# Kernel tuning notes

Measured on AMD Instinct MI355X. Metric: run time of the kernel, lower is better.

Reference implementation:

```python
import jax, jax.numpy as jnp
import numpy as np


def _lap_mul(A, x):
    # L @ x with L = D^{-1/2} A D^{-1/2}, D = diag(rowsum(A))
    d = 1.0 / jnp.sqrt(jnp.sum(A, axis=-1))  # [N]
    return d[:, None] * (A @ (d[:, None] * x))


def setup_inputs() -> dict:
    key = jax.random.key(0)
    k1, k2, k3, k4, k5, k6 = jax.random.split(key, 6)
    N, D_IN, D_OUT = 4096, 128, 128
    x = jax.random.normal(k1, (N, D_IN), dtype=jnp.float32)
    A = jax.random.uniform(k2, (N, N), dtype=jnp.float32)
    # linear params stored as [in, out] (apply via x @ W + b)
    s1 = 1.0 / np.sqrt(D_IN)
    W1 = jax.random.uniform(k3, (D_IN, D_OUT), minval=-s1, maxval=s1, dtype=jnp.float32)
    b1 = jax.random.uniform(k4, (D_OUT,), minval=-s1, maxval=s1, dtype=jnp.float32)
    W2 = jax.random.uniform(k5, (D_IN, D_OUT), minval=-s1, maxval=s1, dtype=jnp.float32)
    b2 = jax.random.uniform(k6, (D_OUT,), minval=-s1, maxval=s1, dtype=jnp.float32)
    return {"x": x, "A": A, "W1": W1, "b1": b1, "W2": W2, "b2": b2, "sigma": 1, "k": 4}


def reference(x, A, W1, b1, W2, b2, sigma, k):
    # first graph conv + linear1 + leaky relu
    z = _lap_mul(A, x) @ W1 + b1            # [N, d_out]
    z = jax.nn.leaky_relu(z, negative_slope=0.1)

    # pairwise Euclidean distance (efficient cdist form, same math as the
    # original broadcasted (z_i - z_j)**2 sum, without the d x N x N blowup)
    sq = jnp.sum(z * z, axis=-1)            # [N]
    d2 = sq[:, None] + sq[None, :] - 2.0 * (z @ z.T)
    d2 = jnp.maximum(d2, 0.0)
    S = jnp.sqrt(d2 + 1e-10)                # [N, N]
    S = jnp.exp(-S / (2.0 * sigma))

    # double-argsort rank -> keep top-k per row (emulates original masking)
    order = jnp.argsort(-S, axis=-1)
    ranks = jnp.argsort(order, axis=-1)
    S = jnp.where(ranks < k, S, 0.0)

    A2 = S + A
    out = _lap_mul(A2, x) @ W2 + b2         # [N, d_out]
    return out
```

## Files before the change

kernel.cpp:

```cpp
#include <hip/hip_runtime.h>
#include <cstdint>
#include <cstddef>

#define NN 4096
#define DD 128

using short8 = __attribute__((ext_vector_type(8))) short;
using f32x4  = __attribute__((ext_vector_type(4))) float;
typedef unsigned long long u64;

typedef __attribute__((address_space(1))) void gvoid;
typedef __attribute__((address_space(3))) void lvoid;

__device__ __forceinline__ void async16(const void* g, void* l) {
  __builtin_amdgcn_global_load_lds((gvoid*)g, (lvoid*)l, 16, 0, 0);
}

__device__ __forceinline__ float dec_f(const void* p) {
  if (!p) return 1.0f;
  int b = *(const int*)p;
  return (b >= 0 && b < 1000000) ? (float)b : __int_as_float(b);
}
__device__ __forceinline__ int dec_i(const void* p) {
  if (!p) return 4;
  int b = *(const int*)p;
  return (b >= 0 && b < 1000000) ? b : (int)__int_as_float(b);
}

__device__ __forceinline__ unsigned short f2bf(float f) {
  union { float f; unsigned int u; } v; v.f = f;
  unsigned int u = v.u;
  unsigned int r = (u + 0x7fffu + ((u >> 16) & 1u)) >> 16;
  return (unsigned short)r;
}

__device__ __forceinline__ void ins4(u64 (&l)[4], u64 k) {
#pragma unroll
  for (int t = 0; t < 4; ++t) {
    u64 old = l[t];
    bool bt = k < old;
    l[t] = bt ? k : old;
    k = bt ? old : k;
  }
}

template <int ROWS, int KC, int NTHR>
__device__ __forceinline__ void stage2(const unsigned short* src, int row0, int kb,
                                       unsigned short* dst, int tid, int stride) {
  const int CPR = KC / 8;
  const int ITER = (ROWS * CPR) / NTHR;
#pragma unroll
  for (int t = 0; t < ITER; ++t) {
    int id = tid + t * NTHR;
    int r = id / CPR;
    int p = id % CPR;
    int lc = p ^ (r & 7);
    const void* g = src + (size_t)(row0 + r) * stride + kb + lc * 8;
    async16(g, dst + (size_t)(id & ~63) * 8);
  }
}

template <int CPR>
__device__ __forceinline__ short8 fragN(const unsigned short* t, int row, int ch) {
  return *(const short8*)(t + (size_t)(row * CPR + (ch ^ (row & 7))) * 8);
}

__global__ __launch_bounds__(256) void k_rowsum_scale(
    const float* __restrict__ A, float* __restrict__ rowsumA,
    float* __restrict__ dvec, unsigned short* __restrict__ Ah) {
  int row = blockIdx.x;
  int tid = threadIdx.x;
  const float4* Arow = (const float4*)(A + (size_t)row * NN);
  float s = 0.f;
#pragma unroll
  for (int l = 0; l < 4; ++l) {
    int idx = tid + l * 256;
    float4 v = Arow[idx];
    s += (v.x + v.y) + (v.z + v.w);
    ushort4 h = {f2bf(v.x), f2bf(v.y), f2bf(v.z), f2bf(v.w)};
    *(ushort4*)(Ah + (size_t)row * NN + idx * 4) = h;
  }
  __shared__ float red[256];
  red[tid] = s;
  __syncthreads();
  if (tid < 64) {
    s = red[tid] + red[tid + 64] + red[tid + 128] + red[tid + 192];
#pragma unroll
    for (int off = 32; off > 0; off >>= 1) s += __shfl_down(s, off, 64);
    if (tid == 0) { rowsumA[row] = s; dvec[row] = rsqrtf(s); }
  }
}

__global__ __launch_bounds__(256) void k_xwt(
    const float* __restrict__ x, const float* __restrict__ scale,
    const float* __restrict__ W, float* __restrict__ U,
    unsigned short* __restrict__ UTh) {
  int r0 = blockIdx.x * 16, tid = threadIdx.x;
  int tr = tid >> 4, tc = tid & 15;
  __shared__ float Xs[16 * 132];
  __shared__ float Ws[32 * 128];
  __shared__ unsigned short Ts[128 * 16];
  __shared__ float ssc[16];
  if (tid < 16) ssc[tid] = scale[r0 + tid];
  __syncthreads();
#pragma unroll
  for (int l = 0; l < 2; ++l) {
    int idx = tid + l * 256;
    int r = idx >> 5, c4 = (idx & 31) << 2;
    float4 xv = *(const float4*)(x + (size_t)(r0 + r) * DD + c4);
    float sc = ssc[r];
    float4 o = {sc * xv.x, sc * xv.y, sc * xv.z, sc * xv.w};
    *(float4*)(Xs + r * 132 + c4) = o;
  }
  float acc[8];
#pragma unroll
  for (int u = 0; u < 8; ++u) acc[u] = 0.f;
  for (int t0 = 0; t0 < 128; t0 += 32) {
    __syncthreads();
#pragma unroll
    for (int l = 0; l < 4; ++l) {
      int idx = tid + l * 256;
      int tt = idx >> 5, c4 = (idx & 31) << 2;
      *(float4*)(Ws + tt * 128 + c4) = *(const float4*)(W + (size_t)(t0 + tt) * DD + c4);
    }
    __syncthreads();
#pragma unroll 8
    for (int tt = 0; tt < 32; ++tt) {
      float g = Xs[tr * 132 + t0 + tt];
      float4 w0 = *(const float4*)(Ws + tt * 128 + tc * 8);
      float4 w1 = *(const float4*)(Ws + tt * 128 + tc * 8 + 4);
      acc[0] = fmaf(g, w0.x, acc[0]); acc[1] = fmaf(g, w0.y, acc[1]);
      acc[2] = fmaf(g, w0.z, acc[2]); acc[3] = fmaf(g, w0.w, acc[3]);
      acc[4] = fmaf(g, w1.x, acc[4]); acc[5] = fmaf(g, w1.y, acc[5]);
      acc[6] = fmaf(g, w1.z, acc[6]); acc[7] = fmaf(g, w1.w, acc[7]);
    }
  }
  if (U) {
    size_t off = (size_t)(r0 + tr) * DD + tc * 8;
    float4 o0 = {acc[0], acc[1], acc[2], acc[3]};
    float4 o1 = {acc[4], acc[5], acc[6], acc[7]};
    *(float4*)(U + off) = o0;
    *(float4*)(U + off + 4) = o1;
  }
#pragma unroll
  for (int j = 0; j < 8; ++j) Ts[(tc * 8 + j) * 16 + tr] = f2bf(acc[j]);
  __syncthreads();
  {
    int row = tid >> 1, h = tid & 1;
    *(short8*)(UTh + (size_t)row * NN + r0 + h * 8) = *(const short8*)(Ts + row * 16 + h * 8);
  }
}

__global__ __launch_bounds__(256) void k_mxwt(
    const u64* __restrict__ pkey, const float* __restrict__ rowsumA,
    const float* __restrict__ x, const float* __restrict__ W,
    float* __restrict__ sval, int* __restrict__ sidx, float* __restrict__ d2vec,
    float* __restrict__ U, unsigned short* __restrict__ UTh,
    const void* kptr, const void* sigptr) {
  int r0 = blockIdx.x * 16, tid = threadIdx.x;
  int tr = tid >> 4, tc = tid & 15;
  __shared__ float Xs[16 * 132];
  __shared__ float Ws[32 * 128];
  __shared__ unsigned short Ts[128 * 16];
  __shared__ u64 mk[256][4];
  __shared__ float ds[16];

  {
    int r = tid >> 4, p = tid & 15;
    const u64* src = pkey + ((size_t)(r0 + r) * 16 + p) * 4;
    ulonglong2 k0 = *(const ulonglong2*)src;
    ulonglong2 k1 = *(const ulonglong2*)(src + 2);
    mk[tid][0] = k0.x; mk[tid][1] = k0.y; mk[tid][2] = k1.x; mk[tid][3] = k1.y;
  }
  __syncthreads();
#pragma unroll
  for (int s = 8; s > 0; s >>= 1) {
    int p = tid & 15;
    if (p < s) {
      u64 b[4] = {mk[tid][0], mk[tid][1], mk[tid][2], mk[tid][3]};
#pragma unroll
      for (int q = 0; q < 4; ++q) ins4(b, mk[tid + s][q]);
      mk[tid][0] = b[0]; mk[tid][1] = b[1]; mk[tid][2] = b[2]; mk[tid][3] = b[3];
    }
    __syncthreads();
  }
  if ((tid & 15) == 0) {
    int rl = tid >> 4;
    int r = r0 + rl;
    int kk = dec_i(kptr); kk = kk < 1 ? 1 : (kk > 4 ? 4 : kk);
    float inv2s = 0.5f / dec_f(sigptr);
    float srw = 0.f;
#pragma unroll
    for (int s = 0; s < 4; ++s) {
      if (s < kk) {
        u64 key = mk[tid][s];
        float d2 = __uint_as_float((unsigned)(key >> 32));
        float S = __expf(-sqrtf(d2 + 1e-10f) * inv2s);
        sval[r * 8 + s] = S;
        sidx[r * 8 + s] = (int)(key & 0xffffffffu);
        srw += S;
      }
    }
    float dd = rsqrtf(rowsumA[r] + srw);
    d2vec[r] = dd;
    ds[rl] = dd;
  }
  __syncthreads();

#pragma unroll
  for (int l = 0; l < 2; ++l) {
    int idx = tid + l * 256;
    int r = idx >> 5, c4 = (idx & 31) << 2;
    float4 xv = *(const float4*)(x + (size_t)(r0 + r) * DD + c4);
    float sc = ds[r];
    float4 o = {sc * xv.x, sc * xv.y, sc * xv.z, sc * xv.w};
    *(float4*)(Xs + r * 132 + c4) = o;
  }
  float acc[8];
#pragma unroll
  for (int u = 0; u < 8; ++u) acc[u] = 0.f;
  for (int t0 = 0; t0 < 128; t0 += 32) {
    __syncthreads();
#pragma unroll
    for (int l = 0; l < 4; ++l) {
      int idx = tid + l * 256;
      int tt = idx >> 5, c4 = (idx & 31) << 2;
      *(float4*)(Ws + tt * 128 + c4) = *(const float4*)(W + (size_t)(t0 + tt) * DD + c4);
    }
    __syncthreads();
#pragma unroll 8
    for (int tt = 0; tt < 32; ++tt) {
      float g = Xs[tr * 132 + t0 + tt];
      float4 w0 = *(const float4*)(Ws + tt * 128 + tc * 8);
      float4 w1 = *(const float4*)(Ws + tt * 128 + tc * 8 + 4);
      acc[0] = fmaf(g, w0.x, acc[0]); acc[1] = fmaf(g, w0.y, acc[1]);
      acc[2] = fmaf(g, w0.z, acc[2]); acc[3] = fmaf(g, w0.w, acc[3]);
      acc[4] = fmaf(g, w1.x, acc[4]); acc[5] = fmaf(g, w1.y, acc[5]);
      acc[6] = fmaf(g, w1.z, acc[6]); acc[7] = fmaf(g, w1.w, acc[7]);
    }
  }
  {
    size_t off = (size_t)(r0 + tr) * DD + tc * 8;
    float4 o0 = {acc[0], acc[1], acc[2], acc[3]};
    float4 o1 = {acc[4], acc[5], acc[6], acc[7]};
    *(float4*)(U + off) = o0;
    *(float4*)(U + off + 4) = o1;
  }
#pragma unroll
  for (int j = 0; j < 8; ++j) Ts[(tc * 8 + j) * 16 + tr] = f2bf(acc[j]);
  __syncthreads();
  {
    int row = tid >> 1, h = tid & 1;
    *(short8*)(UTh + (size_t)row * NN + r0 + h * 8) = *(const short8*)(Ts + row * 16 + h * 8);
  }
}

template <int SPLIT>
__global__ __launch_bounds__(256) void k_gemm_bf16(
    const unsigned short* __restrict__ Ah, const unsigned short* __restrict__ Bh,
    float* __restrict__ G) {
  __shared__ __align__(16) unsigned short As_h[128 * 64];
  __shared__ __align__(16) unsigned short Bs_h[128 * 64];

  int bx = blockIdx.x;
  int mt = bx / SPLIT, sp = bx % SPLIT;
  int m0 = mt * 128;
  const int KLEN = NN / SPLIT;
  int ks = sp * KLEN;
  int tid = threadIdx.x, lane = tid & 63, w = tid >> 6;
  int wm = w >> 1, wn = w & 1;
  int l15 = lane & 15, quad = lane >> 4;

  f32x4 acc[4][4];
#pragma unroll
  for (int a = 0; a < 4; ++a)
#pragma unroll
    for (int b = 0; b < 4; ++b) acc[a][b] = (f32x4){0.f, 0.f, 0.f, 0.f};

  for (int kt = 0; kt < KLEN; kt += 64) {
    int kb = ks + kt;
    __syncthreads();
    stage2<128, 64, 256>(Ah, m0, kb, As_h, tid, NN);
    stage2<128, 64, 256>(Bh, 0, kb, Bs_h, tid, NN);
    __syncthreads();
#pragma unroll
    for (int k0 = 0; k0 < 64; k0 += 32) {
      int ch = (k0 >> 3) + quad;
      short8 a_h[4], b_h[4];
#pragma unroll
      for (int f = 0; f < 4; ++f) {
        a_h[f] = fragN<8>(As_h, wm * 64 + f * 16 + l15, ch);
        b_h[f] = fragN<8>(Bs_h, wn * 64 + f * 16 + l15, ch);
      }
#pragma unroll
      for (int fm = 0; fm < 4; ++fm)
#pragma unroll
        for (int fn = 0; fn < 4; ++fn)
          acc[fm][fn] = __builtin_amdgcn_mfma_f32_16x16x32_bf16(a_h[fm], b_h[fn], acc[fm][fn], 0, 0, 0);
    }
  }
  float* Gp = G + (size_t)sp * NN * DD;
#pragma unroll
  for (int fm = 0; fm < 4; ++fm) {
    int rb = m0 + wm * 64 + fm * 16 + quad * 4;
#pragma unroll
    for (int fn = 0; fn < 4; ++fn) {
      int c = wn * 64 + fn * 16 + l15;
#pragma unroll
      for (int i = 0; i < 4; ++i)
        Gp[(size_t)(rb + i) * DD + c] = acc[fm][fn][i];
    }
  }
}

template <int NP>
__global__ __launch_bounds__(256) void k_red(
    const float* __restrict__ G, const float* __restrict__ dvec,
    const float* __restrict__ bvec, int leaky,
    float* __restrict__ Out, unsigned short* __restrict__ zh,
    float* __restrict__ sqout,
    const float* __restrict__ Usp, const float* __restrict__ sval,
    const int* __restrict__ sidx, const void* kptr) {
  int r0 = blockIdx.x * 16;
  int tid = threadIdx.x;
  int tr = tid >> 4, tc = tid & 15;
  int r = r0 + tr;
  size_t off = (size_t)r * DD + tc * 8;
  __shared__ float red[256];

  float acc[8];
#pragma unroll
  for (int u = 0; u < 8; ++u) acc[u] = 0.f;
#pragma unroll
  for (int p = 0; p < NP; ++p) {
    const float* gp = G + (size_t)p * NN * DD + off;
    float4 g0 = *(const float4*)gp;
    float4 g1 = *(const float4*)(gp + 4);
    acc[0] += g0.x; acc[1] += g0.y; acc[2] += g0.z; acc[3] += g0.w;
    acc[4] += g1.x; acc[5] += g1.y; acc[6] += g1.z; acc[7] += g1.w;
  }
  if (sidx != nullptr) {
    int kk = dec_i(kptr); kk = kk < 1 ? 1 : (kk > 4 ? 4 : kk);
    for (int t = 0; t < kk; ++t) {
      float sv = sval[r * 8 + t];
      int id = sidx[r * 8 + t];
      const float* vr = Usp + (size_t)id * DD + tc * 8;
      float4 w0 = *(const float4*)vr;
      float4 w1 = *(const float4*)(vr + 4);
      acc[0] = fmaf(sv, w0.x, acc[0]); acc[1] = fmaf(sv, w0.y, acc[1]);
      acc[2] = fmaf(sv, w0.z, acc[2]); acc[3] = fmaf(sv, w0.w, acc[3]);
      acc[4] = fmaf(sv, w1.x, acc[4]); acc[5] = fmaf(sv, w1.y, acc[5]);
      acc[6] = fmaf(sv, w1.z, acc[6]); acc[7] = fmaf(sv, w1.w, acc[7]);
    }
  }
  float d = dvec[r];
  float4 b0 = *(const float4*)(bvec + tc * 8);
  float4 b1 = *(const float4*)(bvec + tc * 8 + 4);
  float bb[8] = {b0.x, b0.y, b0.z, b0.w, b1.x, b1.y, b1.z, b1.w};
  float o[8];
#pragma unroll
  for (int u = 0; u < 8; ++u) {
    float v = fmaf(d, acc[u], bb[u]);
    if (leaky) v = v > 0.f ? v : 0.1f * v;
    o[u] = v;
  }
  if (Out) {
    float4 o0 = {o[0], o[1], o[2], o[3]};
    float4 o1 = {o[4], o[5], o[6], o[7]};
    *(float4*)(Out + off) = o0;
    *(float4*)(Out + off + 4) = o1;
  }
  if (zh) {
    ushort4 h0 = {f2bf(o[0]), f2bf(o[1]), f2bf(o[2]), f2bf(o[3])};
    ushort4 h1 = {f2bf(o[4]), f2bf(o[5]), f2bf(o[6]), f2bf(o[7])};
    *(ushort4*)(zh + off) = h0;
    *(ushort4*)(zh + off + 4) = h1;
  }
  if (sqout != nullptr) {
    float p = 0.f;
#pragma unroll
    for (int u = 0; u < 8; ++u) p = fmaf(o[u], o[u], p);
    red[tid] = p;
    __syncthreads();
    if (tc == 0) {
      float s = 0.f;
#pragma unroll
      for (int i = 0; i < 16; ++i) s += red[tr * 16 + i];
      sqout[r] = s;
    }
  }
}

__global__ __launch_bounds__(512, 8) void k_scores(
    const unsigned short* __restrict__ Zh,
    const float* __restrict__ sq, u64* __restrict__ pkey) {
  __shared__ __align__(16) unsigned short Am[64 * 128];
  __shared__ __align__(16) unsigned short Bj[64 * 128];
  float* Stile = (float*)&Bj[0];
  u64* mv = (u64*)&Am[0];

  int bx = blockIdx.x;
  int mt = bx >> 4, jp = bx & 15;
  int m0 = mt * 64, j0 = jp * 256;
  int tid = threadIdx.x, lane = tid & 63, w = tid >> 6;
  int wm = w >> 2, wn = w & 3;
  int l15 = lane & 15, quad = lane >> 4;

  stage2<64, 128, 512>(Zh, m0, 0, Am, tid, DD);

  int srow = tid >> 3;
  int sc = tid & 7;
  float sqi_r = sq[m0 + srow];

  u64 lst[4];
#pragma unroll
  for (int s = 0; s < 4; ++s) lst[s] = ~0ull;

  for (int jt = 0; jt < 4; ++jt) {
    int jrow0 = j0 + jt * 64;
    __syncthreads();
    stage2<64, 128, 512>(Zh, jrow0, 0, Bj, tid, DD);
    __syncthreads();

    f32x4 acc[2];
    acc[0] = (f32x4){0.f, 0.f, 0.f, 0.f};
    acc[1] = (f32x4){0.f, 0.f, 0.f, 0.f};
#pragma unroll
    for (int kc = 0; kc < 4; ++kc) {
      int ch = kc * 4 + quad;
      short8 ah0 = fragN<16>(Am, wm * 32 + l15, ch);
      short8 ah1 = fragN<16>(Am, wm * 32 + 16 + l15, ch);
      short8 bh  = fragN<16>(Bj, wn * 16 + l15, ch);
      acc[0] = __builtin_amdgcn_mfma_f32_16x16x32_bf16(ah0, bh, acc[0], 0, 0, 0);
      acc[1] = __builtin_amdgcn_mfma_f32_16x16x32_bf16(ah1, bh, acc[1], 0, 0, 0);
    }
    __syncthreads();

    {
      int c = wn * 16 + l15;
      float sqjv = sq[jrow0 + c];
      int cslot = c >> 2, cw = c & 3;
#pragma unroll
      for (int fm = 0; fm < 2; ++fm) {
        int rb = wm * 32 + fm * 16 + quad * 4;
#pragma unroll
        for (int i = 0; i < 4; ++i) {
          int r = rb + i;
          Stile[r * 64 + ((cslot ^ (r & 7)) << 2) + cw] = fmaf(-2.f, acc[fm][i], sqjv);
        }
      }
    }
    __syncthreads();

#pragma unroll
    for (int q = 0; q < 2; ++q) {
      int slot = sc * 2 + q;
      float4 kv = *(const float4*)(Stile + srow * 64 + ((slot ^ (srow & 7)) << 2));
      int jb = jrow0 + sc * 8 + q * 4;
      float ke[4] = {kv.x, kv.y, kv.z, kv.w};
#pragma unroll
      for (int e = 0; e < 4; ++e) {
        float v = fmaxf(sqi_r + ke[e], 0.f);
        ins4(lst, ((u64)__float_as_uint(v) << 32) | (unsigned)(jb + e));
      }
    }
  }

  __syncthreads();
#pragma unroll
  for (int s = 0; s < 4; ++s) mv[tid * 4 + s] = lst[s];
  __syncthreads();
  if (tid < 64) {
    u64 best[4] = {~0ull, ~0ull, ~0ull, ~0ull};
    for (int g = 0; g < 8; ++g) {
      int src = tid * 8 + g;
#pragma unroll
      for (int s = 0; s < 4; ++s) ins4(best, mv[src * 4 + s]);
    }
#pragma unroll
    for (int s = 0; s < 4; ++s)
      pkey[((size_t)(m0 + tid) * 16 + jp) * 4 + s] = best[s];
  }
}

extern "C" void kernel_launch(void* const* d_in, const int* in_sizes, int n_in,
                              void* d_out, int out_size, void* d_ws, size_t ws_size,
                              hipStream_t stream) {
  const float* x  = (const float*)d_in[0];
  const float* A  = (const float*)d_in[1];
  const float* W1 = (const float*)d_in[2];
  const float* b1 = (const float*)d_in[3];
  const float* W2 = (const float*)d_in[4];
  const float* b2 = (const float*)d_in[5];
  const void* sig = (n_in > 6) ? d_in[6] : nullptr;
  const void* kp  = (n_in > 7) ? d_in[7] : nullptr;

  float* ws = (float*)d_ws;
  float* rowsumA = ws;
  float* dvec    = ws + 4096;
  float* d2vec   = ws + 8192;
  float* sqv     = ws + 12288;
  float* sval    = ws + 16384;
  int*   sidx    = (int*)(ws + 49152);
  u64*   pkey    = (u64*)(ws + 81920);
  unsigned short* Zh  = (unsigned short*)(ws + 606208);
  float* U       = ws + 868352;
  unsigned short* UTh = (unsigned short*)(ws + 1392640);
  unsigned short* Ah  = (unsigned short*)(ws + 1654784);
  float* G       = ws + 10043392;

  const size_t F16 = 10043392 + 16 * 524288;
  int split16 = (ws_size >= F16 * 4);

  k_rowsum_scale<<<4096, 256, 0, stream>>>(A, rowsumA, dvec, Ah);
  k_xwt<<<256, 256, 0, stream>>>(x, dvec, W1, nullptr, UTh);
  if (split16) {
    k_gemm_bf16<16><<<512, 256, 0, stream>>>(Ah, UTh, G);
    k_red<16><<<256, 256, 0, stream>>>(G, dvec, b1, 1, nullptr, Zh, sqv,
                                       nullptr, nullptr, nullptr, nullptr);
  } else {
    k_gemm_bf16<4><<<128, 256, 0, stream>>>(Ah, UTh, G);
    k_red<4><<<256, 256, 0, stream>>>(G, dvec, b1, 1, nullptr, Zh, sqv,
                                      nullptr, nullptr, nullptr, nullptr);
  }
  k_scores<<<1024, 512, 0, stream>>>(Zh, sqv, pkey);
  k_mxwt<<<256, 256, 0, stream>>>(pkey, rowsumA, x, W2, sval, sidx, d2vec,
                                  U, UTh, kp, sig);
  if (split16) {
    k_gemm_bf16<16><<<512, 256, 0, stream>>>(Ah, UTh, G);
    k_red<16><<<256, 256, 0, stream>>>(G, d2vec, b2, 0, (float*)d_out, nullptr, nullptr,
                                       U, sval, sidx, kp);
  } else {
    k_gemm_bf16<4><<<128, 256, 0, stream>>>(Ah, UTh, G);
    k_red<4><<<256, 256, 0, stream>>>(G, d2vec, b2, 0, (float*)d_out, nullptr, nullptr,
                                      U, sval, sidx, kp);
  }
}
```

Measured before the change: 199.0 us.

## Fuse split-K reduction into GEMM via last-block counter and prune top-k inserts

Merges the split-K partial-sum reduction and epilogue (scaling, bias, leaky relu, bf16 output, squared norms, sparse top-k contribution) into the GEMM kernel. The last block per row tile, detected with an atomic counter, does the reduction, which removes two kernel launches and their gaps. Counters are zeroed inside the row-sum kernel. The scores kernel also skips top-4 insertion when a candidate exceeds the current fourth-best key. The tradeoff is that the reduction now runs on only 32 blocks, serialised behind the tail of the GEMM.

```diff
diff --git a/kernel.cpp b/kernel.cpp
--- a/kernel.cpp
+++ b/kernel.cpp
@@ -67,9 +67,11 @@
 
 __global__ __launch_bounds__(256) void k_rowsum_scale(
     const float* __restrict__ A, float* __restrict__ rowsumA,
-    float* __restrict__ dvec, unsigned short* __restrict__ Ah) {
+    float* __restrict__ dvec, unsigned short* __restrict__ Ah,
+    int* __restrict__ cnt) {
   int row = blockIdx.x;
   int tid = threadIdx.x;
+  if (row == 0 && tid < 128) cnt[tid] = 0;
   const float4* Arow = (const float4*)(A + (size_t)row * NN);
   float s = 0.f;
 #pragma unroll
@@ -256,11 +258,18 @@
 }
 
 template <int SPLIT>
-__global__ __launch_bounds__(256) void k_gemm_bf16(
+__global__ __launch_bounds__(256) void k_gemm_fused(
     const unsigned short* __restrict__ Ah, const unsigned short* __restrict__ Bh,
-    float* __restrict__ G) {
+    float* __restrict__ G, int* __restrict__ cnt,
+    const float* __restrict__ dvec, const float* __restrict__ bvec, int leaky,
+    float* __restrict__ Out, unsigned short* __restrict__ zh,
+    float* __restrict__ sqout,
+    const float* __restrict__ Usp, const float* __restrict__ sval,
+    const int* __restrict__ sidx, const void* kptr) {
   __shared__ __align__(16) unsigned short As_h[128 * 64];
   __shared__ __align__(16) unsigned short Bs_h[128 * 64];
+  __shared__ float redsh[256];
+  __shared__ int islast;
 
   int bx = blockIdx.x;
   int mt = bx / SPLIT, sp = bx % SPLIT;
@@ -299,94 +308,95 @@
           acc[fm][fn] = __builtin_amdgcn_mfma_f32_16x16x32_bf16(a_h[fm], b_h[fn], acc[fm][fn], 0, 0, 0);
     }
   }
-  float* Gp = G + (size_t)sp * NN * DD;
-#pragma unroll
-  for (int fm = 0; fm < 4; ++fm) {
-    int rb = m0 + wm * 64 + fm * 16 + quad * 4;
-#pragma unroll
-    for (int fn = 0; fn < 4; ++fn) {
-      int c = wn * 64 + fn * 16 + l15;
-#pragma unroll
-      for (int i = 0; i < 4; ++i)
-        Gp[(size_t)(rb + i) * DD + c] = acc[fm][fn][i];
-    }
-  }
-}
-
-template <int NP>
-__global__ __launch_bounds__(256) void k_red(
-    const float* __restrict__ G, const float* __restrict__ dvec,
-    const float* __restrict__ bvec, int leaky,
-    float* __restrict__ Out, unsigned short* __restrict__ zh,
-    float* __restrict__ sqout,
-    const float* __restrict__ Usp, const float* __restrict__ sval,
-    const int* __restrict__ sidx, const void* kptr) {
-  int r0 = blockIdx.x * 16;
-  int tid = threadIdx.x;
+  {
+    float* Gp = G + (size_t)sp * NN * DD;
+#pragma unroll
+    for (int fm = 0; fm < 4; ++fm) {
+      int rb = m0 + wm * 64 + fm * 16 + quad * 4;
+#pragma unroll
+      for (int fn = 0; fn < 4; ++fn) {
+        int c = wn * 64 + fn * 16 + l15;
+#pragma unroll
+        for (int i = 0; i < 4; ++i)
+          Gp[(size_t)(rb + i) * DD + c] = acc[fm][fn][i];
+      }
+    }
+  }
+
+  __threadfence();
+  __syncthreads();
+  if (tid == 0) islast = (atomicAdd(&cnt[mt], 1) == SPLIT - 1);
+  __syncthreads();
+  if (!islast) return;
+  __threadfence();
+
+  int kk = 0;
+  if (sidx != nullptr) { kk = dec_i(kptr); kk = kk < 1 ? 1 : (kk > 4 ? 4 : kk); }
   int tr = tid >> 4, tc = tid & 15;
-  int r = r0 + tr;
-  size_t off = (size_t)r * DD + tc * 8;
-  __shared__ float red[256];
-
-  float acc[8];
-#pragma unroll
-  for (int u = 0; u < 8; ++u) acc[u] = 0.f;
-#pragma unroll
-  for (int p = 0; p < NP; ++p) {
-    const float* gp = G + (size_t)p * NN * DD + off;
-    float4 g0 = *(const float4*)gp;
-    float4 g1 = *(const float4*)(gp + 4);
-    acc[0] += g0.x; acc[1] += g0.y; acc[2] += g0.z; acc[3] += g0.w;
-    acc[4] += g1.x; acc[5] += g1.y; acc[6] += g1.z; acc[7] += g1.w;
-  }
-  if (sidx != nullptr) {
-    int kk = dec_i(kptr); kk = kk < 1 ? 1 : (kk > 4 ? 4 : kk);
-    for (int t = 0; t < kk; ++t) {
-      float sv = sval[r * 8 + t];
-      int id = sidx[r * 8 + t];
-      const float* vr = Usp + (size_t)id * DD + tc * 8;
-      float4 w0 = *(const float4*)vr;
-      float4 w1 = *(const float4*)(vr + 4);
-      acc[0] = fmaf(sv, w0.x, acc[0]); acc[1] = fmaf(sv, w0.y, acc[1]);
-      acc[2] = fmaf(sv, w0.z, acc[2]); acc[3] = fmaf(sv, w0.w, acc[3]);
-      acc[4] = fmaf(sv, w1.x, acc[4]); acc[5] = fmaf(sv, w1.y, acc[5]);
-      acc[6] = fmaf(sv, w1.z, acc[6]); acc[7] = fmaf(sv, w1.w, acc[7]);
-    }
-  }
-  float d = dvec[r];
-  float4 b0 = *(const float4*)(bvec + tc * 8);
-  float4 b1 = *(const float4*)(bvec + tc * 8 + 4);
-  float bb[8] = {b0.x, b0.y, b0.z, b0.w, b1.x, b1.y, b1.z, b1.w};
-  float o[8];
-#pragma unroll
-  for (int u = 0; u < 8; ++u) {
-    float v = fmaf(d, acc[u], bb[u]);
-    if (leaky) v = v > 0.f ? v : 0.1f * v;
-    o[u] = v;
-  }
-  if (Out) {
-    float4 o0 = {o[0], o[1], o[2], o[3]};
-    float4 o1 = {o[4], o[5], o[6], o[7]};
-    *(float4*)(Out + off) = o0;
-    *(float4*)(Out + off + 4) = o1;
-  }
-  if (zh) {
-    ushort4 h0 = {f2bf(o[0]), f2bf(o[1]), f2bf(o[2]), f2bf(o[3])};
-    ushort4 h1 = {f2bf(o[4]), f2bf(o[5]), f2bf(o[6]), f2bf(o[7])};
-    *(ushort4*)(zh + off) = h0;
-    *(ushort4*)(zh + off + 4) = h1;
-  }
-  if (sqout != nullptr) {
-    float p = 0.f;
-#pragma unroll
-    for (int u = 0; u < 8; ++u) p = fmaf(o[u], o[u], p);
-    red[tid] = p;
-    __syncthreads();
-    if (tc == 0) {
-      float s = 0.f;
-#pragma unroll
-      for (int i = 0; i < 16; ++i) s += red[tr * 16 + i];
-      sqout[r] = s;
+#pragma unroll 1
+  for (int sub = 0; sub < 8; ++sub) {
+    int r = m0 + sub * 16 + tr;
+    size_t off = (size_t)r * DD + tc * 8;
+    float acc2[8];
+#pragma unroll
+    for (int u = 0; u < 8; ++u) acc2[u] = 0.f;
+#pragma unroll
+    for (int p = 0; p < SPLIT; ++p) {
+      const float* gp = G + (size_t)p * NN * DD + off;
+      float4 g0 = *(const float4*)gp;
+      float4 g1 = *(const float4*)(gp + 4);
+      acc2[0] += g0.x; acc2[1] += g0.y; acc2[2] += g0.z; acc2[3] += g0.w;
+      acc2[4] += g1.x; acc2[5] += g1.y; acc2[6] += g1.z; acc2[7] += g1.w;
+    }
+    if (sidx != nullptr) {
+      for (int t = 0; t < kk; ++t) {
+        float sv = sval[r * 8 + t];
+        int id = sidx[r * 8 + t];
+        const float* vr = Usp + (size_t)id * DD + tc * 8;
+        float4 w0 = *(const float4*)vr;
+        float4 w1 = *(const float4*)(vr + 4);
+        acc2[0] = fmaf(sv, w0.x, acc2[0]); acc2[1] = fmaf(sv, w0.y, acc2[1]);
+        acc2[2] = fmaf(sv, w0.z, acc2[2]); acc2[3] = fmaf(sv, w0.w, acc2[3]);
+        acc2[4] = fmaf(sv, w1.x, acc2[4]); acc2[5] = fmaf(sv, w1.y, acc2[5]);
+        acc2[6] = fmaf(sv, w1.z, acc2[6]); acc2[7] = fmaf(sv, w1.w, acc2[7]);
+      }
+    }
+    float d = dvec[r];
+    float4 b0 = *(const float4*)(bvec + tc * 8);
+    float4 b1 = *(const float4*)(bvec + tc * 8 + 4);
+    float bb[8] = {b0.x, b0.y, b0.z, b0.w, b1.x, b1.y, b1.z, b1.w};
+    float o[8];
+#pragma unroll
+    for (int u = 0; u < 8; ++u) {
+      float v = fmaf(d, acc2[u], bb[u]);
+      if (leaky) v = v > 0.f ? v : 0.1f * v;
+      o[u] = v;
+    }
+    if (Out) {
+      float4 o0 = {o[0], o[1], o[2], o[3]};
+      float4 o1 = {o[4], o[5], o[6], o[7]};
+      *(float4*)(Out + off) = o0;
+      *(float4*)(Out + off + 4) = o1;
+    }
+    if (zh) {
+      ushort4 h0 = {f2bf(o[0]), f2bf(o[1]), f2bf(o[2]), f2bf(o[3])};
+      ushort4 h1 = {f2bf(o[4]), f2bf(o[5]), f2bf(o[6]), f2bf(o[7])};
+      *(ushort4*)(zh + off) = h0;
+      *(ushort4*)(zh + off + 4) = h1;
+    }
+    if (sqout != nullptr) {
+      float p = 0.f;
+#pragma unroll
+      for (int u = 0; u < 8; ++u) p = fmaf(o[u], o[u], p);
+      redsh[tid] = p;
+      __syncthreads();
+      if (tc == 0) {
+        float s = 0.f;
+#pragma unroll
+        for (int i = 0; i < 16; ++i) s += redsh[tr * 16 + i];
+        sqout[r] = s;
+      }
+      __syncthreads();
     }
   }
 }
@@ -415,6 +425,7 @@
   u64 lst[4];
 #pragma unroll
   for (int s = 0; s < 4; ++s) lst[s] = ~0ull;
+  unsigned cutb = 0xffffffffu;
 
   for (int jt = 0; jt < 4; ++jt) {
     int jrow0 = j0 + jt * 64;
@@ -461,7 +472,11 @@
 #pragma unroll
       for (int e = 0; e < 4; ++e) {
         float v = fmaxf(sqi_r + ke[e], 0.f);
-        ins4(lst, ((u64)__float_as_uint(v) << 32) | (unsigned)(jb + e));
+        unsigned vb = __float_as_uint(v);
+        if (vb <= cutb) {
+          ins4(lst, ((u64)vb << 32) | (unsigned)(jb + e));
+          cutb = (unsigned)(lst[3] >> 32);
+        }
       }
     }
   }
@@ -500,39 +515,40 @@
   float* dvec    = ws + 4096;
   float* d2vec   = ws + 8192;
   float* sqv     = ws + 12288;
-  float* sval    = ws + 16384;
-  int*   sidx    = (int*)(ws + 49152);
-  u64*   pkey    = (u64*)(ws + 81920);
-  unsigned short* Zh  = (unsigned short*)(ws + 606208);
-  float* U       = ws + 868352;
-  unsigned short* UTh = (unsigned short*)(ws + 1392640);
-  unsigned short* Ah  = (unsigned short*)(ws + 1654784);
-  float* G       = ws + 10043392;
-
-  const size_t F16 = 10043392 + 16 * 524288;
+  int*   cnt     = (int*)(ws + 16384);
+  float* sval    = ws + 16512;
+  int*   sidx    = (int*)(ws + 49280);
+  u64*   pkey    = (u64*)(ws + 82048);
+  unsigned short* Zh  = (unsigned short*)(ws + 606336);
+  float* U       = ws + 868480;
+  unsigned short* UTh = (unsigned short*)(ws + 1392768);
+  unsigned short* Ah  = (unsigned short*)(ws + 1654912);
+  float* G       = ws + 10043520;
+
+  const size_t F16 = 10043520 + 16 * 524288;
   int split16 = (ws_size >= F16 * 4);
 
-  k_rowsum_scale<<<4096, 256, 0, stream>>>(A, rowsumA, dvec, Ah);
+  k_rowsum_scale<<<4096, 256, 0, stream>>>(A, rowsumA, dvec, Ah, cnt);
   k_xwt<<<256, 256, 0, stream>>>(x, dvec, W1, nullptr, UTh);
   if (split16) {
-    k_gemm_bf16<16><<<512, 256, 0, stream>>>(Ah, UTh, G);
-    k_red<16><<<256, 256, 0, stream>>>(G, dvec, b1, 1, nullptr, Zh, sqv,
-                                       nullptr, nullptr, nullptr, nullptr);
+    k_gemm_fused<16><<<512, 256, 0, stream>>>(Ah, UTh, G, cnt, dvec, b1, 1,
+                                              nullptr, Zh, sqv,
+                                              nullptr, nullptr, nullptr, nullptr);
   } else {
-    k_gemm_bf16<4><<<128, 256, 0, stream>>>(Ah, UTh, G);
-    k_red<4><<<256, 256, 0, stream>>>(G, dvec, b1, 1, nullptr, Zh, sqv,
-                                      nullptr, nullptr, nullptr, nullptr);
+    k_gemm_fused<4><<<128, 256, 0, stream>>>(Ah, UTh, G, cnt, dvec, b1, 1,
+                                             nullptr, Zh, sqv,
+                                             nullptr, nullptr, nullptr, nullptr);
   }
   k_scores<<<1024, 512, 0, stream>>>(Zh, sqv, pkey);
   k_mxwt<<<256, 256, 0, stream>>>(pkey, rowsumA, x, W2, sval, sidx, d2vec,
                                   U, UTh, kp, sig);
   if (split16) {
-    k_gemm_bf16<16><<<512, 256, 0, stream>>>(Ah, UTh, G);
-    k_red<16><<<256, 256, 0, stream>>>(G, d2vec, b2, 0, (float*)d_out, nullptr, nullptr,
-                                       U, sval, sidx, kp);
+    k_gemm_fused<16><<<512, 256, 0, stream>>>(Ah, UTh, G, cnt + 64, d2vec, b2, 0,
+                                              (float*)d_out, nullptr, nullptr,
+                                              U, sval, sidx, kp);
   } else {
-    k_gemm_bf16<4><<<128, 256, 0, stream>>>(Ah, UTh, G);
-    k_red<4><<<256, 256, 0, stream>>>(G, d2vec, b2, 0, (float*)d_out, nullptr, nullptr,
-                                      U, sval, sidx, kp);
-  }
-}
+    k_gemm_fused<4><<<128, 256, 0, stream>>>(Ah, UTh, G, cnt + 64, d2vec, b2, 0,
+                                             (float*)d_out, nullptr, nullptr,
+                                             U, sval, sidx, kp);
+  }
+}
```

Measured after the change: 423.8 us. +113.0%, slower.

## Fuse split-K GEMM and reduction into one full-K row-tile kernel

Applied to the files above, without the earlier changes.

Replaces the split-K bf16 GEMM plus separate reduction kernel with a single kernel. Each block owns 16 rows, walks the full K=4096 with 8 waves each covering 16 output columns, and applies the epilogue (degree scaling, bias, leaky relu, bf16 store, squared norms, sparse top-k add) directly from shared memory. This drops the large fp32 partial-sum buffer traffic and one launch per pass. In exchange each block reloads the whole 128-wide B tile every K step, the kernel runs only 256 blocks with a long serial K loop and one MFMA chain per wave, and partial sums are flushed from the MFMA accumulator every two steps.

```diff
diff --git a/kernel.cpp b/kernel.cpp
--- a/kernel.cpp
+++ b/kernel.cpp
@@ -255,137 +255,113 @@
   }
 }
 
-template <int SPLIT>
-__global__ __launch_bounds__(256) void k_gemm_bf16(
+template <int PASS>
+__global__ __launch_bounds__(512) void k_gr(
     const unsigned short* __restrict__ Ah, const unsigned short* __restrict__ Bh,
-    float* __restrict__ G) {
-  __shared__ __align__(16) unsigned short As_h[128 * 64];
-  __shared__ __align__(16) unsigned short Bs_h[128 * 64];
-
-  int bx = blockIdx.x;
-  int mt = bx / SPLIT, sp = bx % SPLIT;
-  int m0 = mt * 128;
-  const int KLEN = NN / SPLIT;
-  int ks = sp * KLEN;
-  int tid = threadIdx.x, lane = tid & 63, w = tid >> 6;
-  int wm = w >> 1, wn = w & 1;
-  int l15 = lane & 15, quad = lane >> 4;
-
-  f32x4 acc[4][4];
-#pragma unroll
-  for (int a = 0; a < 4; ++a)
-#pragma unroll
-    for (int b = 0; b < 4; ++b) acc[a][b] = (f32x4){0.f, 0.f, 0.f, 0.f};
-
-  for (int kt = 0; kt < KLEN; kt += 64) {
-    int kb = ks + kt;
-    __syncthreads();
-    stage2<128, 64, 256>(Ah, m0, kb, As_h, tid, NN);
-    stage2<128, 64, 256>(Bh, 0, kb, Bs_h, tid, NN);
-    __syncthreads();
-#pragma unroll
-    for (int k0 = 0; k0 < 64; k0 += 32) {
-      int ch = (k0 >> 3) + quad;
-      short8 a_h[4], b_h[4];
-#pragma unroll
-      for (int f = 0; f < 4; ++f) {
-        a_h[f] = fragN<8>(As_h, wm * 64 + f * 16 + l15, ch);
-        b_h[f] = fragN<8>(Bs_h, wn * 64 + f * 16 + l15, ch);
-      }
-#pragma unroll
-      for (int fm = 0; fm < 4; ++fm)
-#pragma unroll
-        for (int fn = 0; fn < 4; ++fn)
-          acc[fm][fn] = __builtin_amdgcn_mfma_f32_16x16x32_bf16(a_h[fm], b_h[fn], acc[fm][fn], 0, 0, 0);
-    }
-  }
-  float* Gp = G + (size_t)sp * NN * DD;
-#pragma unroll
-  for (int fm = 0; fm < 4; ++fm) {
-    int rb = m0 + wm * 64 + fm * 16 + quad * 4;
-#pragma unroll
-    for (int fn = 0; fn < 4; ++fn) {
-      int c = wn * 64 + fn * 16 + l15;
-#pragma unroll
-      for (int i = 0; i < 4; ++i)
-        Gp[(size_t)(rb + i) * DD + c] = acc[fm][fn][i];
-    }
-  }
-}
-
-template <int NP>
-__global__ __launch_bounds__(256) void k_red(
-    const float* __restrict__ G, const float* __restrict__ dvec,
-    const float* __restrict__ bvec, int leaky,
+    const float* __restrict__ dvec, const float* __restrict__ bvec,
     float* __restrict__ Out, unsigned short* __restrict__ zh,
     float* __restrict__ sqout,
     const float* __restrict__ Usp, const float* __restrict__ sval,
     const int* __restrict__ sidx, const void* kptr) {
-  int r0 = blockIdx.x * 16;
-  int tid = threadIdx.x;
+  __shared__ __align__(16) unsigned short As_h[16 * 128];
+  __shared__ __align__(16) unsigned short Bs_h[128 * 128];
+  float* osh   = (float*)&Bs_h[0];
+  float* redsh = (float*)&As_h[0];
+
+  int bx = blockIdx.x;
+  int r0 = bx * 16;
+  int tid = threadIdx.x, lane = tid & 63, w = tid >> 6;
+  int l15 = lane & 15, quad = lane >> 4;
+  int c = w * 16 + l15;
+
+  f32x4 run = (f32x4){0.f, 0.f, 0.f, 0.f};
+  f32x4 ck  = (f32x4){0.f, 0.f, 0.f, 0.f};
+
+  for (int kt = 0; kt < 32; ++kt) {
+    int kb = kt * 128;
+    __syncthreads();
+    if (tid < 256) {
+      int r = tid >> 4, p = tid & 15;
+      int lc = p ^ (r & 7);
+      async16(Ah + (size_t)(r0 + r) * NN + kb + lc * 8,
+              (unsigned short*)As_h + (size_t)(tid & ~63) * 8);
+    }
+    stage2<128, 128, 512>(Bh, 0, kb, Bs_h, tid, NN);
+    __syncthreads();
+#pragma unroll
+    for (int kc = 0; kc < 4; ++kc) {
+      int ch = kc * 4 + quad;
+      short8 a_h = fragN<16>(As_h, l15, ch);
+      short8 b_h = fragN<16>(Bs_h, w * 16 + l15, ch);
+      ck = __builtin_amdgcn_mfma_f32_16x16x32_bf16(a_h, b_h, ck, 0, 0, 0);
+    }
+    if (kt & 1) {
+      run[0] += ck[0]; run[1] += ck[1]; run[2] += ck[2]; run[3] += ck[3];
+      ck = (f32x4){0.f, 0.f, 0.f, 0.f};
+    }
+  }
+
+  __syncthreads();
+#pragma unroll
+  for (int i = 0; i < 4; ++i) osh[(quad * 4 + i) * 128 + c] = run[i];
+  __syncthreads();
+
   int tr = tid >> 4, tc = tid & 15;
   int r = r0 + tr;
   size_t off = (size_t)r * DD + tc * 8;
-  __shared__ float red[256];
-
-  float acc[8];
-#pragma unroll
-  for (int u = 0; u < 8; ++u) acc[u] = 0.f;
-#pragma unroll
-  for (int p = 0; p < NP; ++p) {
-    const float* gp = G + (size_t)p * NN * DD + off;
-    float4 g0 = *(const float4*)gp;
-    float4 g1 = *(const float4*)(gp + 4);
-    acc[0] += g0.x; acc[1] += g0.y; acc[2] += g0.z; acc[3] += g0.w;
-    acc[4] += g1.x; acc[5] += g1.y; acc[6] += g1.z; acc[7] += g1.w;
-  }
-  if (sidx != nullptr) {
-    int kk = dec_i(kptr); kk = kk < 1 ? 1 : (kk > 4 ? 4 : kk);
-    for (int t = 0; t < kk; ++t) {
-      float sv = sval[r * 8 + t];
-      int id = sidx[r * 8 + t];
-      const float* vr = Usp + (size_t)id * DD + tc * 8;
-      float4 w0 = *(const float4*)vr;
-      float4 w1 = *(const float4*)(vr + 4);
-      acc[0] = fmaf(sv, w0.x, acc[0]); acc[1] = fmaf(sv, w0.y, acc[1]);
-      acc[2] = fmaf(sv, w0.z, acc[2]); acc[3] = fmaf(sv, w0.w, acc[3]);
-      acc[4] = fmaf(sv, w1.x, acc[4]); acc[5] = fmaf(sv, w1.y, acc[5]);
-      acc[6] = fmaf(sv, w1.z, acc[6]); acc[7] = fmaf(sv, w1.w, acc[7]);
-    }
-  }
-  float d = dvec[r];
-  float4 b0 = *(const float4*)(bvec + tc * 8);
-  float4 b1 = *(const float4*)(bvec + tc * 8 + 4);
-  float bb[8] = {b0.x, b0.y, b0.z, b0.w, b1.x, b1.y, b1.z, b1.w};
-  float o[8];
-#pragma unroll
-  for (int u = 0; u < 8; ++u) {
-    float v = fmaf(d, acc[u], bb[u]);
-    if (leaky) v = v > 0.f ? v : 0.1f * v;
-    o[u] = v;
-  }
-  if (Out) {
-    float4 o0 = {o[0], o[1], o[2], o[3]};
-    float4 o1 = {o[4], o[5], o[6], o[7]};
-    *(float4*)(Out + off) = o0;
-    *(float4*)(Out + off + 4) = o1;
-  }
-  if (zh) {
-    ushort4 h0 = {f2bf(o[0]), f2bf(o[1]), f2bf(o[2]), f2bf(o[3])};
-    ushort4 h1 = {f2bf(o[4]), f2bf(o[5]), f2bf(o[6]), f2bf(o[7])};
-    *(ushort4*)(zh + off) = h0;
-    *(ushort4*)(zh + off + 4) = h1;
-  }
-  if (sqout != nullptr) {
-    float p = 0.f;
-#pragma unroll
-    for (int u = 0; u < 8; ++u) p = fmaf(o[u], o[u], p);
-    red[tid] = p;
-    __syncthreads();
-    if (tc == 0) {
+  float p2 = 0.f;
+  if (tid < 256) {
+    float acc[8];
+#pragma unroll
+    for (int u = 0; u < 8; ++u) acc[u] = osh[tr * 128 + tc * 8 + u];
+    if (PASS == 2 && sidx != nullptr) {
+      int kk = dec_i(kptr); kk = kk < 1 ? 1 : (kk > 4 ? 4 : kk);
+      for (int t = 0; t < kk; ++t) {
+        float sv = sval[r * 8 + t];
+        int id = sidx[r * 8 + t];
+        const float* vr = Usp + (size_t)id * DD + tc * 8;
+        float4 w0 = *(const float4*)vr;
+        float4 w1 = *(const float4*)(vr + 4);
+        acc[0] = fmaf(sv, w0.x, acc[0]); acc[1] = fmaf(sv, w0.y, acc[1]);
+        acc[2] = fmaf(sv, w0.z, acc[2]); acc[3] = fmaf(sv, w0.w, acc[3]);
+        acc[4] = fmaf(sv, w1.x, acc[4]); acc[5] = fmaf(sv, w1.y, acc[5]);
+        acc[6] = fmaf(sv, w1.z, acc[6]); acc[7] = fmaf(sv, w1.w, acc[7]);
+      }
+    }
+    float d = dvec[r];
+    float4 b0 = *(const float4*)(bvec + tc * 8);
+    float4 b1 = *(const float4*)(bvec + tc * 8 + 4);
+    float bb[8] = {b0.x, b0.y, b0.z, b0.w, b1.x, b1.y, b1.z, b1.w};
+    float o[8];
+#pragma unroll
+    for (int u = 0; u < 8; ++u) {
+      float v = fmaf(d, acc[u], bb[u]);
+      if (PASS == 1) v = v > 0.f ? v : 0.1f * v;
+      o[u] = v;
+    }
+    if (PASS == 2) {
+      float4 o0 = {o[0], o[1], o[2], o[3]};
+      float4 o1 = {o[4], o[5], o[6], o[7]};
+      *(float4*)(Out + off) = o0;
+      *(float4*)(Out + off + 4) = o1;
+    }
+    if (PASS == 1) {
+      ushort4 h0 = {f2bf(o[0]), f2bf(o[1]), f2bf(o[2]), f2bf(o[3])};
+      ushort4 h1 = {f2bf(o[4]), f2bf(o[5]), f2bf(o[6]), f2bf(o[7])};
+      *(ushort4*)(zh + off) = h0;
+      *(ushort4*)(zh + off + 4) = h1;
+#pragma unroll
+      for (int u = 0; u < 8; ++u) p2 = fmaf(o[u], o[u], p2);
+    }
+  }
+  if (PASS == 1) {
+    __syncthreads();
+    if (tid < 256) redsh[tid] = p2;
+    __syncthreads();
+    if (tid < 256 && tc == 0) {
       float s = 0.f;
 #pragma unroll
-      for (int i = 0; i < 16; ++i) s += red[tr * 16 + i];
+      for (int i = 0; i < 16; ++i) s += redsh[tr * 16 + i];
       sqout[r] = s;
     }
   }
@@ -507,32 +483,14 @@
   float* U       = ws + 868352;
   unsigned short* UTh = (unsigned short*)(ws + 1392640);
   unsigned short* Ah  = (unsigned short*)(ws + 1654784);
-  float* G       = ws + 10043392;
-
-  const size_t F16 = 10043392 + 16 * 524288;
-  int split16 = (ws_size >= F16 * 4);
 
   k_rowsum_scale<<<4096, 256, 0, stream>>>(A, rowsumA, dvec, Ah);
   k_xwt<<<256, 256, 0, stream>>>(x, dvec, W1, nullptr, UTh);
-  if (split16) {
-    k_gemm_bf16<16><<<512, 256, 0, stream>>>(Ah, UTh, G);
-    k_red<16><<<256, 256, 0, stream>>>(G, dvec, b1, 1, nullptr, Zh, sqv,
-                                       nullptr, nullptr, nullptr, nullptr);
-  } else {
-    k_gemm_bf16<4><<<128, 256, 0, stream>>>(Ah, UTh, G);
-    k_red<4><<<256, 256, 0, stream>>>(G, dvec, b1, 1, nullptr, Zh, sqv,
-                                      nullptr, nullptr, nullptr, nullptr);
-  }
+  k_gr<1><<<256, 512, 0, stream>>>(Ah, UTh, dvec, b1, nullptr, Zh, sqv,
+                                   nullptr, nullptr, nullptr, nullptr);
   k_scores<<<1024, 512, 0, stream>>>(Zh, sqv, pkey);
   k_mxwt<<<256, 256, 0, stream>>>(pkey, rowsumA, x, W2, sval, sidx, d2vec,
                                   U, UTh, kp, sig);
-  if (split16) {
-    k_gemm_bf16<16><<<512, 256, 0, stream>>>(Ah, UTh, G);
-    k_red<16><<<256, 256, 0, stream>>>(G, d2vec, b2, 0, (float*)d_out, nullptr, nullptr,
-                                       U, sval, sidx, kp);
-  } else {
-    k_gemm_bf16<4><<<128, 256, 0, stream>>>(Ah, UTh, G);
-    k_red<4><<<256, 256, 0, stream>>>(G, d2vec, b2, 0, (float*)d_out, nullptr, nullptr,
-                                      U, sval, sidx, kp);
-  }
-}
+  k_gr<2><<<256, 512, 0, stream>>>(Ah, UTh, d2vec, b2, (float*)d_out, nullptr, nullptr,
+                                   U, sval, sidx, kp);
+}
```

Measured after the change: 226.4 us. 1.14x slower.
